# Performance work log

Hardware: AMD Instinct MI355X
Metric: run time of the kernel (lower is better)

Reference implementation:

```python
import jax, jax.numpy as jnp
import numpy as np

B, T, C = 2, 2048, 2048
N_HEAD, N_KV_HEAD, HEAD_DIM = 16, 4, 128
N_REP = N_HEAD // N_KV_HEAD
EPS = 1e-05


def setup_inputs() -> dict:
    key = jax.random.key(0)
    ks = jax.random.split(key, 8)
    # rope freqs as cos/sin of theta_t,i = t / 10000^(2i/d)
    inv_freq = 1.0 / (10000.0 ** (np.arange(0, HEAD_DIM, 2, dtype=np.float32) / HEAD_DIM))
    ang = np.arange(T, dtype=np.float32)[:, None] * inv_freq[None, :]  # [T, HEAD_DIM//2]
    scale = 0.02
    return {
        "x": jax.random.normal(ks[0], (B, T, C), jnp.float32),
        "freqs_cos": jnp.asarray(np.cos(ang)),
        "freqs_sin": jnp.asarray(np.sin(ang)),
        "wq": jax.random.normal(ks[1], (C, N_HEAD * HEAD_DIM), jnp.float32) * scale,
        "wk": jax.random.normal(ks[2], (C, N_KV_HEAD * HEAD_DIM), jnp.float32) * scale,
        "wv": jax.random.normal(ks[3], (C, N_KV_HEAD * HEAD_DIM), jnp.float32) * scale,
        "wo": jax.random.normal(ks[4], (N_HEAD * HEAD_DIM, C), jnp.float32) * scale,
        "q_norm_w": jnp.ones((HEAD_DIM,), jnp.float32),
        "k_norm_w": jnp.ones((HEAD_DIM,), jnp.float32),
    }


def _rmsnorm(x, w):
    var = jnp.mean(jnp.square(x), axis=-1, keepdims=True)
    return x * jax.lax.rsqrt(var + EPS) * w


def _rope(x, cos, sin):
    # x: [B, T, H, D]; interpret last dim as interleaved (real, imag) pairs
    xr = x[..., 0::2]
    xi = x[..., 1::2]
    c = cos[None, :, None, :]
    s = sin[None, :, None, :]
    out_r = xr * c - xi * s
    out_i = xr * s + xi * c
    return jnp.stack([out_r, out_i], axis=-1).reshape(x.shape)


def reference(x, freqs_cos, freqs_sin, wq, wk, wv, wo, q_norm_w, k_norm_w):
    # QKV projections
    xq = (x @ wq).reshape(B, T, N_HEAD, HEAD_DIM)
    xk = (x @ wk).reshape(B, T, N_KV_HEAD, HEAD_DIM)
    xv = (x @ wv).reshape(B, T, N_KV_HEAD, HEAD_DIM)
    # optional q/k RMSNorm (use_qk_norm=True)
    xq = _rmsnorm(xq, q_norm_w)
    xk = _rmsnorm(xk, k_norm_w)
    # RoPE
    xq = _rope(xq, freqs_cos, freqs_sin)
    xk = _rope(xk, freqs_cos, freqs_sin)
    # GQA expand: each kv head repeated N_REP times contiguously
    xk = jnp.repeat(xk, N_REP, axis=2)  # [B, T, N_HEAD, D]
    xv = jnp.repeat(xv, N_REP, axis=2)
    # causal SDPA
    scores = jnp.einsum("bthd,bshd->bhts", xq, xk) / jnp.sqrt(jnp.float32(HEAD_DIM))
    causal = jnp.tril(jnp.ones((T, T), bool))
    scores = jnp.where(causal[None, None], scores, jnp.float32(-1e30))
    attn = jax.nn.softmax(scores, axis=-1)
    y = jnp.einsum("bhts,bshd->bthd", attn, xv).reshape(B, T, N_HEAD * HEAD_DIM)
    return y @ wo
```

## Files before the change

### kernel.cpp

```cpp
#include <hip/hip_runtime.h>
#include <hip/hip_bf16.h>

using u16 = unsigned short;
using u32 = unsigned int;

typedef short bf16x8 __attribute__((ext_vector_type(8)));
typedef float f32x4 __attribute__((ext_vector_type(4)));

#define AS1 __attribute__((address_space(1)))
#define AS3 __attribute__((address_space(3)))

__device__ __forceinline__ void gll16(const void* g, void* l) {
  __builtin_amdgcn_global_load_lds((const AS1 u32*)g, (AS3 u32*)l, 16, 0, 0);
}

__device__ __forceinline__ u16 f2bf(float x) {
  u32 u = __builtin_bit_cast(u32, x);
  u32 r = (u + 0x7fffu + ((u >> 16) & 1u)) >> 16;
  return (u16)r;
}
__device__ __forceinline__ u32 pk2(float lo, float hi) {
  return (u32)f2bf(lo) | ((u32)f2bf(hi) << 16);
}
__device__ __forceinline__ u16 f2bf_fast(float x) {
  __hip_bfloat16 h = __float2bfloat16(x);
  return __builtin_bit_cast(u16, h);
}

__device__ __forceinline__ void trans64(const float* __restrict__ in, u16* __restrict__ out,
                                        int R, int Cc, int bx, int by, float (*tl)[65]) {
  int c0 = bx * 64, r0 = by * 64, tid = threadIdx.x;
#pragma unroll
  for (int i = 0; i < 16; i++) {
    int idx = i * 256 + tid; int tr = idx >> 6, tc = idx & 63;
    tl[tr][tc] = in[(size_t)(r0 + tr) * Cc + c0 + tc];
  }
  __syncthreads();
#pragma unroll
  for (int i = 0; i < 16; i++) {
    int idx = i * 256 + tid; int tr = idx >> 6, tc = idx & 63;
    out[(size_t)(c0 + tr) * R + r0 + tc] = f2bf(tl[tc][tr]);
  }
}

__global__ void k_prep(const float* __restrict__ x, u16* __restrict__ xb,
                       const float* __restrict__ wq, u16* __restrict__ wqt,
                       const float* __restrict__ wk, const float* __restrict__ wv,
                       u16* __restrict__ wkvt,
                       const float* __restrict__ wo, u16* __restrict__ wot,
                       const float* __restrict__ fc, const float* __restrict__ fs,
                       float2* __restrict__ fcs) {
  __shared__ float tl[64][65];
  int gid = blockIdx.x;
  if (gid < 4096) {
    int i = gid * 256 + threadIdx.x;
    const float4* p = (const float4*)(x + (size_t)i * 8);
    float4 a = p[0], b = p[1];
    uint4 o;
    o.x = pk2(a.x, a.y); o.y = pk2(a.z, a.w);
    o.z = pk2(b.x, b.y); o.w = pk2(b.z, b.w);
    *(uint4*)(xb + (size_t)i * 8) = o;
  } else if (gid < 5120) {
    int t = gid - 4096; trans64(wq, wqt, 2048, 2048, t & 31, t >> 5, tl);
  } else if (gid < 5376) {
    int t = gid - 5120; trans64(wk, wkvt, 2048, 512, t & 7, t >> 3, tl);
  } else if (gid < 5632) {
    int t = gid - 5376; trans64(wv, wkvt + 512 * 2048, 2048, 512, t & 7, t >> 3, tl);
  } else if (gid < 6656) {
    int t = gid - 5632; trans64(wo, wot, 2048, 2048, t & 31, t >> 5, tl);
  } else {
    int base = (gid - 6656) * 2048 + threadIdx.x * 8;
#pragma unroll
    for (int j = 0; j < 8; j++) {
      int idx = base + j;
      fcs[idx] = make_float2(fc[idx], fs[idx]);
    }
  }
}

__global__ __launch_bounds__(512, 2) void k_gemm_qkv(
    const u16* __restrict__ A, const u16* __restrict__ BT0, const u16* __restrict__ BT1,
    u16* __restrict__ Qout, u16* __restrict__ Kout, u16* __restrict__ Vout,
    const float* __restrict__ nwq, const float* __restrict__ nwk,
    const float2* __restrict__ fcs) {
  __shared__ char lds[147456];
  const int K = 2048;
  int tid = threadIdx.x, w = tid >> 6, l = tid & 63, lg = l >> 4, ll = l & 15;
  int bid = blockIdx.x;

  if (bid < 256) {
    int wr = w >> 2, wc = w & 3;
    int xcd = bid & 7, r = bid >> 3;
    int colg = xcd & 1, rowg = xcd >> 1;
    int bxt = colg * 4 + (r & 3);
    int bm0 = (rowg * 8 + (r >> 2)) * 128;
    int bn0 = bxt * 256;

    auto stage = [&](int si, int kt) {
      char* Sb = lds + si * 49152;
      int k0 = kt * 64;
#pragma unroll
      for (int i = 0; i < 2; i++) {
        int base = i * 512 + (w << 6);
        int c = base + l;
        int row = c >> 3, kc = (c & 7) ^ (row & 7);
        gll16(A + (size_t)(bm0 + row) * K + k0 + kc * 8, Sb + base * 16);
      }
#pragma unroll
      for (int i = 0; i < 4; i++) {
        int base = i * 512 + (w << 6);
        int c = base + l;
        int row = c >> 3, kc = (c & 7) ^ (row & 7);
        gll16(BT0 + (size_t)(bn0 + row) * K + k0 + kc * 8, Sb + 16384 + base * 16);
      }
    };

    f32x4 acc[4][4] = {};
    stage(0, 0); stage(1, 1);
    asm volatile("s_waitcnt vmcnt(6)" ::: "memory");
    __builtin_amdgcn_s_barrier();
    __builtin_amdgcn_sched_barrier(0);

    for (int kt = 0; kt < 32; ++kt) {
      int cs = kt % 3;
      if (kt + 2 < 32) stage((kt + 2) % 3, kt + 2);
      char* As = lds + cs * 49152;
      char* Bs = As + 16384;
      __builtin_amdgcn_s_setprio(1);
#pragma unroll
      for (int ks = 0; ks < 2; ks++) {
        bf16x8 af[4], bf[4];
#pragma unroll
        for (int m = 0; m < 4; m++) {
          int row = 64 * wr + 16 * m + ll;
          af[m] = *(const bf16x8*)(As + row * 128 + (((lg + 4 * ks) ^ (row & 7)) << 4));
        }
#pragma unroll
        for (int n = 0; n < 4; n++) {
          int row = 64 * wc + 16 * n + ll;
          bf[n] = *(const bf16x8*)(Bs + row * 128 + (((lg + 4 * ks) ^ (row & 7)) << 4));
        }
#pragma unroll
        for (int m = 0; m < 4; m++)
#pragma unroll
          for (int n = 0; n < 4; n++)
            acc[m][n] = __builtin_amdgcn_mfma_f32_16x16x32_bf16(af[m], bf[n], acc[m][n], 0, 0, 0);
      }
      __builtin_amdgcn_s_setprio(0);
      if (kt + 2 < 32) {
        asm volatile("s_waitcnt vmcnt(6)" ::: "memory");
      } else {
        asm volatile("s_waitcnt vmcnt(0)" ::: "memory");
      }
      __builtin_amdgcn_s_barrier();
      __builtin_amdgcn_sched_barrier(0);
    }

    float* ssum = (float*)lds;
    float ps[4][4];
#pragma unroll
    for (int m = 0; m < 4; m++)
#pragma unroll
      for (int r2 = 0; r2 < 4; r2++) {
        float p = 0.f;
#pragma unroll
        for (int n = 0; n < 4; n++) p += acc[m][n][r2] * acc[m][n][r2];
#pragma unroll
        for (int msk = 1; msk < 16; msk <<= 1) p += __shfl_xor(p, msk);
        ps[m][r2] = p;
      }
    if (ll == 0) {
#pragma unroll
      for (int m = 0; m < 4; m++)
#pragma unroll
        for (int r2 = 0; r2 < 4; r2++)
          ssum[wr * 256 + (16 * m + 4 * lg + r2) * 4 + wc] = ps[m][r2];
    }
    __syncthreads();
    int pbase = (wc < 2) ? 0 : 2;
    float rs[4][4];
#pragma unroll
    for (int m = 0; m < 4; m++)
#pragma unroll
      for (int r2 = 0; r2 < 4; r2++) {
        int rowl = 16 * m + 4 * lg + r2;
        const float* sp = ssum + wr * 256 + rowl * 4;
        float tot = sp[pbase] + sp[pbase + 1];
        rs[m][r2] = rsqrtf(tot * (1.0f / 128.0f) + 1e-5f) * 0.12751744843f;
      }
#pragma unroll
    for (int m = 0; m < 4; m++)
#pragma unroll
      for (int n = 0; n < 4; n++) {
        int col = bn0 + 64 * wc + 16 * n + ll;
        int d = col & 127;
        float wgt = nwq[d];
        int i = d >> 1;
#pragma unroll
        for (int r2 = 0; r2 < 4; r2++) {
          int row = bm0 + 64 * wr + 16 * m + 4 * lg + r2;
          int t = row & 2047;
          float y = acc[m][n][r2] * rs[m][r2] * wgt;
          float p = __shfl_xor(y, 1);
          float2 cs2 = fcs[t * 64 + i];
          float o = (ll & 1) ? (p * cs2.y + y * cs2.x) : (y * cs2.x - p * cs2.y);
          Qout[(size_t)row * 2048 + col] = f2bf(o);
        }
      }
  } else {
    int wr = w >> 2, wc = w & 3;
    int lid = bid - 256;
    int xcd = lid & 7, r = lid >> 3;
    int colg = xcd & 1, rowg = xcd >> 1;
    int bxt = colg * 4 + (r & 3);
    int bm0 = (rowg * 8 + (r >> 2)) * 128;
    int bn0 = bxt * 128;
    bool kpath = (bn0 < 512);

    auto stage = [&](int si, int kt) {
      char* Sb = lds + si * 32768;
      int k0 = kt * 64;
#pragma unroll
      for (int i = 0; i < 2; i++) {
        int base = i * 512 + (w << 6);
        int c = base + l;
        int row = c >> 3, kc = (c & 7) ^ (row & 7);
        gll16(A + (size_t)(bm0 + row) * K + k0 + kc * 8, Sb + base * 16);
        gll16(BT1 + (size_t)(bn0 + row) * K + k0 + kc * 8, Sb + 16384 + base * 16);
      }
    };

    f32x4 acc[4][2] = {};
    stage(0, 0); stage(1, 1); stage(2, 2);
    asm volatile("s_waitcnt vmcnt(8)" ::: "memory");
    __builtin_amdgcn_s_barrier();
    __builtin_amdgcn_sched_barrier(0);

    for (int kt = 0; kt < 32; ++kt) {
      int cs = kt & 3;
      if (kt + 3 < 32) stage((kt + 3) & 3, kt + 3);
      char* As = lds + cs * 32768;
      char* Bs = As + 16384;
      __builtin_amdgcn_s_setprio(1);
#pragma unroll
      for (int ks = 0; ks < 2; ks++) {
        bf16x8 af[4], bf[2];
#pragma unroll
        for (int m = 0; m < 4; m++) {
          int row = 64 * wr + 16 * m + ll;
          af[m] = *(const bf16x8*)(As + row * 128 + (((lg + 4 * ks) ^ (row & 7)) << 4));
        }
#pragma unroll
        for (int n = 0; n < 2; n++) {
          int row = 32 * wc + 16 * n + ll;
          bf[n] = *(const bf16x8*)(Bs + row * 128 + (((lg + 4 * ks) ^ (row & 7)) << 4));
        }
#pragma unroll
        for (int m = 0; m < 4; m++)
#pragma unroll
          for (int n = 0; n < 2; n++)
            acc[m][n] = __builtin_amdgcn_mfma_f32_16x16x32_bf16(af[m], bf[n], acc[m][n], 0, 0, 0);
      }
      __builtin_amdgcn_s_setprio(0);
      if (kt <= 28) {
        asm volatile("s_waitcnt vmcnt(8)" ::: "memory");
      } else if (kt == 29) {
        asm volatile("s_waitcnt vmcnt(4)" ::: "memory");
      } else {
        asm volatile("s_waitcnt vmcnt(0)" ::: "memory");
      }
      __builtin_amdgcn_s_barrier();
      __builtin_amdgcn_sched_barrier(0);
    }

    if (kpath) {
      float* ssum = (float*)lds;
      float ps[4][4];
#pragma unroll
      for (int m = 0; m < 4; m++)
#pragma unroll
        for (int r2 = 0; r2 < 4; r2++) {
          float p = 0.f;
#pragma unroll
          for (int n = 0; n < 2; n++) p += acc[m][n][r2] * acc[m][n][r2];
#pragma unroll
          for (int msk = 1; msk < 16; msk <<= 1) p += __shfl_xor(p, msk);
          ps[m][r2] = p;
        }
      if (ll == 0) {
#pragma unroll
        for (int m = 0; m < 4; m++)
#pragma unroll
          for (int r2 = 0; r2 < 4; r2++)
            ssum[wr * 256 + (16 * m + 4 * lg + r2) * 4 + wc] = ps[m][r2];
      }
      __syncthreads();
      float rs[4][4];
#pragma unroll
      for (int m = 0; m < 4; m++)
#pragma unroll
        for (int r2 = 0; r2 < 4; r2++) {
          int rowl = 16 * m + 4 * lg + r2;
          const float* sp = ssum + wr * 256 + rowl * 4;
          float tot = sp[0] + sp[1] + sp[2] + sp[3];
          rs[m][r2] = rsqrtf(tot * (1.0f / 128.0f) + 1e-5f);
        }
#pragma unroll
      for (int m = 0; m < 4; m++)
#pragma unroll
        for (int n = 0; n < 2; n++) {
          int col = bn0 + 32 * wc + 16 * n + ll;
          int d = col & 127;
          float wgt = nwk[d];
          int i = d >> 1;
#pragma unroll
          for (int r2 = 0; r2 < 4; r2++) {
            int row = bm0 + 64 * wr + 16 * m + 4 * lg + r2;
            int t = row & 2047;
            float y = acc[m][n][r2] * rs[m][r2] * wgt;
            float p = __shfl_xor(y, 1);
            float2 cs2 = fcs[t * 64 + i];
            float o = (ll & 1) ? (p * cs2.y + y * cs2.x) : (y * cs2.x - p * cs2.y);
            Kout[(size_t)row * 512 + col] = f2bf(o);
          }
        }
    } else {
      int b = bm0 >> 11, t0g = bm0 & 2047;
      int kvh = (bn0 - 512) >> 7;
      int bk = b * 4 + kvh;
#pragma unroll
      for (int m = 0; m < 4; m++)
#pragma unroll
        for (int n = 0; n < 2; n++) {
          int d = 32 * wc + 16 * n + ll;
          int tloc = 64 * wr + 16 * m + 4 * lg;
          u32 w0 = pk2(acc[m][n][0], acc[m][n][1]);
          u32 w1 = pk2(acc[m][n][2], acc[m][n][3]);
          int byte = (d * 256 + tloc * 2) ^ ((d & 7) << 4);
          *(uint2*)(lds + byte) = make_uint2(w0, w1);
        }
      __syncthreads();
      int tc = tid & 15, dbase = tid >> 4;
#pragma unroll
      for (int pass = 0; pass < 4; pass++) {
        int d = dbase + pass * 32;
        int byte = (d * 256 + tc * 16) ^ ((d & 7) << 4);
        uint4 v = *(const uint4*)(lds + byte);
        *(uint4*)(Vout + ((size_t)(bk * 128 + d)) * 2048 + t0g + tc * 8) = v;
      }
    }
  }
}

__global__ __launch_bounds__(512, 2) void k_gemm_o(
    const u16* __restrict__ A, const u16* __restrict__ BT, float* __restrict__ C) {
  __shared__ char lds[147456];
  const int K = 2048;
  int tid = threadIdx.x, w = tid >> 6, l = tid & 63, lg = l >> 4, ll = l & 15;
  int wr = w >> 2, wc = w & 3;
  int lid = blockIdx.y * 8 + blockIdx.x;
  int xcd = lid & 7, r = lid >> 3;
  int colg = xcd & 1, rowg = xcd >> 1;
  int bxt = colg * 4 + (r & 3);
  int bm0 = (rowg * 8 + (r >> 2)) * 128;
  int bn0 = bxt * 256;

  auto stage = [&](int si, int kt) {
    char* Sb = lds + si * 49152;
    int k0 = kt * 64;
#pragma unroll
    for (int i = 0; i < 2; i++) {
      int base = i * 512 + (w << 6);
      int c = base + l;
      int row = c >> 3, kc = (c & 7) ^ (row & 7);
      gll16(A + (size_t)(bm0 + row) * K + k0 + kc * 8, Sb + base * 16);
    }
#pragma unroll
    for (int i = 0; i < 4; i++) {
      int base = i * 512 + (w << 6);
      int c = base + l;
      int row = c >> 3, kc = (c & 7) ^ (row & 7);
      gll16(BT + (size_t)(bn0 + row) * K + k0 + kc * 8, Sb + 16384 + base * 16);
    }
  };

  f32x4 acc[4][4] = {};
  stage(0, 0); stage(1, 1);
  asm volatile("s_waitcnt vmcnt(6)" ::: "memory");
  __builtin_amdgcn_s_barrier();
  __builtin_amdgcn_sched_barrier(0);

  for (int kt = 0; kt < 32; ++kt) {
    int cs = kt % 3;
    if (kt + 2 < 32) stage((kt + 2) % 3, kt + 2);
    char* As = lds + cs * 49152;
    char* Bs = As + 16384;
    __builtin_amdgcn_s_setprio(1);
#pragma unroll
    for (int ks = 0; ks < 2; ks++) {
      bf16x8 af[4], bf[4];
#pragma unroll
      for (int m = 0; m < 4; m++) {
        int row = 64 * wr + 16 * m + ll;
        af[m] = *(const bf16x8*)(As + row * 128 + (((lg + 4 * ks) ^ (row & 7)) << 4));
      }
#pragma unroll
      for (int n = 0; n < 4; n++) {
        int row = 64 * wc + 16 * n + ll;
        bf[n] = *(const bf16x8*)(Bs + row * 128 + (((lg + 4 * ks) ^ (row & 7)) << 4));
      }
#pragma unroll
      for (int m = 0; m < 4; m++)
#pragma unroll
        for (int n = 0; n < 4; n++)
          acc[m][n] = __builtin_amdgcn_mfma_f32_16x16x32_bf16(af[m], bf[n], acc[m][n], 0, 0, 0);
    }
    __builtin_amdgcn_s_setprio(0);
    if (kt + 2 < 32) {
      asm volatile("s_waitcnt vmcnt(6)" ::: "memory");
    } else {
      asm volatile("s_waitcnt vmcnt(0)" ::: "memory");
    }
    __builtin_amdgcn_s_barrier();
    __builtin_amdgcn_sched_barrier(0);
  }

#pragma unroll
  for (int m = 0; m < 4; m++)
#pragma unroll
    for (int n = 0; n < 4; n++) {
      int row = bm0 + 64 * wr + 16 * m + 4 * lg;
      int col = bn0 + 64 * wc + 16 * n + ll;
      float* cp = C + (size_t)row * 2048 + col;
#pragma unroll
      for (int r2 = 0; r2 < 4; r2++) cp[(size_t)r2 * 2048] = acc[m][n][r2];
    }
}

__global__ __launch_bounds__(512, 2) void k_attn(
    const u16* __restrict__ Q, const u16* __restrict__ Kb,
    const u16* __restrict__ Vt, u16* __restrict__ Y) {
  __shared__ char lds[81920];
  char* Ps = lds + 65536;
  int tid = threadIdx.x, w = tid >> 6, l = tid & 63, lg = l >> 4, ll = l & 15;
  int fid = blockIdx.x;
  int g = fid & 7, rank = fid >> 3;
  int b = g >> 2, kvh = g & 3;
  int h = kvh * 4 + (w & 3);
  int rgrp = w >> 2;
  const u16* Kbase = Kb + ((size_t)b * 2048) * 512 + kvh * 128;
  const u16* Vbase = Vt + ((size_t)(b * 4 + kvh) * 128) * 2048;

  const bf16x8 vones = {(short)0x3F80, (short)0x3F80, (short)0x3F80, (short)0x3F80,
                        (short)0x3F80, (short)0x3F80, (short)0x3F80, (short)0x3F80};

  auto stage = [&](int bi, int k0) {
    char* Kd = lds + (bi ? 32768 : 0);
    char* Vd = Kd + 16384;
#pragma unroll
    for (int i = 0; i < 2; i++) {
      int base = i * 512 + (w << 6);
      int c = base + l;
      int dst = base * 16;
      int krow = c >> 4, ksrc = (c & 15) ^ (krow & 7);
      gll16(Kbase + (size_t)(k0 + krow) * 512 + ksrc * 8, Kd + dst);
      int vd = c >> 3, vsrc = (c & 7) ^ (vd & 7);
      gll16(Vbase + (size_t)vd * 2048 + k0 + vsrc * 8, Vd + dst);
    }
  };

#pragma unroll 1
  for (int qi = 0; qi < 2; qi++) {
    int qt = qi ? (63 - rank) : rank;
    int q0 = qt * 32;
    int nt = (qt >> 1) + 1;
    bf16x8 qf[4];
    {
      int qrow = b * 2048 + q0 + rgrp * 16 + ll;
      const u16* qp = Q + (size_t)qrow * 2048 + h * 128;
#pragma unroll
      for (int ks = 0; ks < 4; ks++) qf[ks] = *(const bf16x8*)(qp + ks * 32 + lg * 8);
    }
    f32x4 o[8] = {};
    f32x4 lacc = {};

    stage(0, 0);
    asm volatile("s_waitcnt vmcnt(0)" ::: "memory");
    __syncthreads();

    int cur = 0;
    for (int it = 0; it < nt; ++it) {
      if (it + 1 < nt) stage(cur ^ 1, (it + 1) * 64);
      char* Ks = lds + (cur ? 32768 : 0);
      char* Vs = Ks + 16384;
      f32x4 s[4] = {};
      __builtin_amdgcn_s_setprio(1);
#pragma unroll
      for (int ks = 0; ks < 4; ks++) {
#pragma unroll
        for (int n = 0; n < 4; n++) {
          int row = 16 * n + ll;
          bf16x8 kf = *(const bf16x8*)(Ks + ((row * 256 + (lg + 4 * ks) * 16) ^ ((row & 7) << 4)));
          s[n] = __builtin_amdgcn_mfma_f32_16x16x32_bf16(qf[ks], kf, s[n], 0, 0, 0);
        }
      }
      __builtin_amdgcn_s_setprio(0);
      if (it == nt - 1) {
        int k0 = it * 64;
#pragma unroll
        for (int n = 0; n < 4; n++) {
          int kk = k0 + 16 * n + ll;
#pragma unroll
          for (int r = 0; r < 4; r++) {
            int qq = q0 + rgrp * 16 + 4 * lg + r;
            if (kk > qq) s[n][r] = -1e30f;
          }
        }
      }
#pragma unroll
      for (int r = 0; r < 4; r++) {
        int prow = 4 * lg + r;
#pragma unroll
        for (int n = 0; n < 4; n++) {
          float e = exp2f(s[n][r]);
          int byte = (w << 11) + ((prow * 128 + (16 * n + ll) * 2) ^ ((prow & 7) << 4));
          *(u16*)(Ps + byte) = f2bf_fast(e);
        }
      }
      __builtin_amdgcn_s_setprio(1);
#pragma unroll
      for (int ks = 0; ks < 2; ks++) {
        bf16x8 pf = *(const bf16x8*)(Ps + (w << 11) + ((ll * 128 + (lg + 4 * ks) * 16) ^ ((ll & 7) << 4)));
        lacc = __builtin_amdgcn_mfma_f32_16x16x32_bf16(pf, vones, lacc, 0, 0, 0);
#pragma unroll
        for (int n = 0; n < 8; n++) {
          int row = 16 * n + ll;
          bf16x8 vf = *(const bf16x8*)(Vs + ((row * 128 + (lg + 4 * ks) * 16) ^ ((row & 7) << 4)));
          o[n] = __builtin_amdgcn_mfma_f32_16x16x32_bf16(pf, vf, o[n], 0, 0, 0);
        }
      }
      __builtin_amdgcn_s_setprio(0);
      asm volatile("s_waitcnt vmcnt(0)" ::: "memory");
      __syncthreads();
      cur ^= 1;
    }
    float rl[4];
#pragma unroll
    for (int r = 0; r < 4; r++) rl[r] = 1.0f / lacc[r];
#pragma unroll
    for (int n = 0; n < 8; n++) {
      int col = h * 128 + 16 * n + ll;
#pragma unroll
      for (int r = 0; r < 4; r++) {
        int trow = b * 2048 + q0 + rgrp * 16 + 4 * lg + r;
        Y[(size_t)trow * 2048 + col] = f2bf_fast(o[n][r] * rl[r]);
      }
    }
  }
}

extern "C" void kernel_launch(void* const* d_in, const int* in_sizes, int n_in,
                              void* d_out, int out_size, void* d_ws, size_t ws_size,
                              hipStream_t stream) {
  const float* x   = (const float*)d_in[0];
  const float* fc  = (const float*)d_in[1];
  const float* fs  = (const float*)d_in[2];
  const float* wq  = (const float*)d_in[3];
  const float* wk  = (const float*)d_in[4];
  const float* wv  = (const float*)d_in[5];
  const float* wo  = (const float*)d_in[6];
  const float* qnw = (const float*)d_in[7];
  const float* knw = (const float*)d_in[8];
  float* out = (float*)d_out;

  const size_t MB = 1ull << 20;
  char* ws = (char*)d_ws;
  u16*    xb   = (u16*)(ws);
  u16*    wqt  = (u16*)(ws + 16 * MB);
  u16*    wkvt = (u16*)(ws + 24 * MB);
  u16*    wot  = (u16*)(ws + 28 * MB);
  u16*    Qb   = (u16*)(ws + 36 * MB);
  u16*    Kbq  = (u16*)(ws + 52 * MB);
  u16*    Vtg  = (u16*)(ws + 56 * MB);
  u16*    Yb   = (u16*)(ws + 60 * MB);
  float2* fcs  = (float2*)(ws + 76 * MB);

  hipLaunchKernelGGL(k_prep, dim3(6720), dim3(256), 0, stream,
                     x, xb, wq, wqt, wk, wv, wkvt, wo, wot, fc, fs, fcs);
  hipLaunchKernelGGL(k_gemm_qkv, dim3(512), dim3(512), 0, stream,
                     xb, wqt, wkvt, Qb, Kbq, Vtg, qnw, knw, fcs);
  hipLaunchKernelGGL(k_attn, dim3(256), dim3(512), 0, stream, Qb, Kbq, Vtg, Yb);
  hipLaunchKernelGGL(k_gemm_o, dim3(8, 32), dim3(512), 0, stream, Yb, wot, out);
}
```

Measured before the change: 186.4 us.

## Restructure attention to 4-wave blocks with 32-row per-wave Q tiles

```diff
diff --git a/kernel.cpp b/kernel.cpp
--- a/kernel.cpp
+++ b/kernel.cpp
@@ -437,29 +437,44 @@
     }
 }
 
-__global__ __launch_bounds__(512, 2) void k_attn(
+__global__ __launch_bounds__(256, 2) void k_attn(
     const u16* __restrict__ Q, const u16* __restrict__ Kb,
     const u16* __restrict__ Vt, u16* __restrict__ Y) {
-  __shared__ char lds[81920];
+  __shared__ char lds[73728];
   char* Ps = lds + 65536;
   int tid = threadIdx.x, w = tid >> 6, l = tid & 63, lg = l >> 4, ll = l & 15;
   int fid = blockIdx.x;
-  int g = fid & 7, rank = fid >> 3;
+  int g = fid & 7;
   int b = g >> 2, kvh = g & 3;
-  int h = kvh * 4 + (w & 3);
-  int rgrp = w >> 2;
+  int hp = (fid >> 3) & 1;
+  int qt = 31 - (fid >> 4);
+  int h = kvh * 4 + hp * 2 + (w & 1);
+  int rgrp = w >> 1;
+  int q0 = qt * 64;
+  int nt = qt + 1;
   const u16* Kbase = Kb + ((size_t)b * 2048) * 512 + kvh * 128;
   const u16* Vbase = Vt + ((size_t)(b * 4 + kvh) * 128) * 2048;
 
   const bf16x8 vones = {(short)0x3F80, (short)0x3F80, (short)0x3F80, (short)0x3F80,
                         (short)0x3F80, (short)0x3F80, (short)0x3F80, (short)0x3F80};
+
+  bf16x8 qf[2][4];
+#pragma unroll
+  for (int m = 0; m < 2; m++) {
+    int qrow = b * 2048 + q0 + rgrp * 32 + m * 16 + ll;
+    const u16* qp = Q + (size_t)qrow * 2048 + h * 128;
+#pragma unroll
+    for (int ks = 0; ks < 4; ks++) qf[m][ks] = *(const bf16x8*)(qp + ks * 32 + lg * 8);
+  }
+  f32x4 o[2][8] = {};
+  f32x4 lacc[2] = {};
 
   auto stage = [&](int bi, int k0) {
     char* Kd = lds + (bi ? 32768 : 0);
     char* Vd = Kd + 16384;
 #pragma unroll
-    for (int i = 0; i < 2; i++) {
-      int base = i * 512 + (w << 6);
+    for (int i = 0; i < 4; i++) {
+      int base = i * 256 + (w << 6);
       int c = base + l;
       int dst = base * 16;
       int krow = c >> 4, ksrc = (c & 15) ^ (krow & 7);
@@ -469,91 +484,92 @@
     }
   };
 
-#pragma unroll 1
-  for (int qi = 0; qi < 2; qi++) {
-    int qt = qi ? (63 - rank) : rank;
-    int q0 = qt * 32;
-    int nt = (qt >> 1) + 1;
-    bf16x8 qf[4];
-    {
-      int qrow = b * 2048 + q0 + rgrp * 16 + ll;
-      const u16* qp = Q + (size_t)qrow * 2048 + h * 128;
-#pragma unroll
-      for (int ks = 0; ks < 4; ks++) qf[ks] = *(const bf16x8*)(qp + ks * 32 + lg * 8);
-    }
-    f32x4 o[8] = {};
-    f32x4 lacc = {};
-
-    stage(0, 0);
+  stage(0, 0);
+  asm volatile("s_waitcnt vmcnt(0)" ::: "memory");
+  __syncthreads();
+
+  int cur = 0;
+  for (int it = 0; it < nt; ++it) {
+    if (it + 1 < nt) stage(cur ^ 1, (it + 1) * 64);
+    char* Ks = lds + (cur ? 32768 : 0);
+    char* Vs = Ks + 16384;
+    f32x4 s[2][4] = {};
+    __builtin_amdgcn_s_setprio(1);
+#pragma unroll
+    for (int ks = 0; ks < 4; ks++) {
+#pragma unroll
+      for (int n = 0; n < 4; n++) {
+        int row = 16 * n + ll;
+        bf16x8 kf = *(const bf16x8*)(Ks + ((row * 256 + (lg + 4 * ks) * 16) ^ ((row & 7) << 4)));
+        s[0][n] = __builtin_amdgcn_mfma_f32_16x16x32_bf16(qf[0][ks], kf, s[0][n], 0, 0, 0);
+        s[1][n] = __builtin_amdgcn_mfma_f32_16x16x32_bf16(qf[1][ks], kf, s[1][n], 0, 0, 0);
+      }
+    }
+    __builtin_amdgcn_s_setprio(0);
+    if (it == nt - 1) {
+      int k0 = it * 64;
+#pragma unroll
+      for (int m = 0; m < 2; m++)
+#pragma unroll
+        for (int n = 0; n < 4; n++) {
+          int kk = k0 + 16 * n + ll;
+#pragma unroll
+          for (int r = 0; r < 4; r++) {
+            int qq = q0 + rgrp * 32 + m * 16 + 4 * lg + r;
+            if (kk > qq) s[m][n][r] = -1e30f;
+          }
+        }
+    }
+#pragma unroll
+    for (int hs = 0; hs < 2; hs++) {
+#pragma unroll
+      for (int m = 0; m < 2; m++)
+#pragma unroll
+        for (int r = 0; r < 4; r++) {
+          int prow = m * 16 + 4 * lg + r;
+          int swz = ((prow >> 2) & 3) << 4;
+#pragma unroll
+          for (int nn = 0; nn < 2; nn++) {
+            int n = 2 * hs + nn;
+            float e = exp2f(s[m][n][r]);
+            int lcol = 16 * nn + ll;
+            int byte = (w << 11) + ((prow * 64 + lcol * 2) ^ swz);
+            *(u16*)(Ps + byte) = f2bf_fast(e);
+          }
+        }
+      __builtin_amdgcn_s_setprio(1);
+      bf16x8 pfm[2];
+#pragma unroll
+      for (int m = 0; m < 2; m++) {
+        int prow = m * 16 + ll;
+        pfm[m] = *(const bf16x8*)(Ps + (w << 11) + ((prow * 64 + lg * 16) ^ (((prow >> 2) & 3) << 4)));
+        lacc[m] = __builtin_amdgcn_mfma_f32_16x16x32_bf16(pfm[m], vones, lacc[m], 0, 0, 0);
+      }
+#pragma unroll
+      for (int n = 0; n < 8; n++) {
+        int row = 16 * n + ll;
+        bf16x8 vf = *(const bf16x8*)(Vs + ((row * 128 + (lg + 4 * hs) * 16) ^ ((row & 7) << 4)));
+        o[0][n] = __builtin_amdgcn_mfma_f32_16x16x32_bf16(pfm[0], vf, o[0][n], 0, 0, 0);
+        o[1][n] = __builtin_amdgcn_mfma_f32_16x16x32_bf16(pfm[1], vf, o[1][n], 0, 0, 0);
+      }
+      __builtin_amdgcn_s_setprio(0);
+    }
     asm volatile("s_waitcnt vmcnt(0)" ::: "memory");
     __syncthreads();
-
-    int cur = 0;
-    for (int it = 0; it < nt; ++it) {
-      if (it + 1 < nt) stage(cur ^ 1, (it + 1) * 64);
-      char* Ks = lds + (cur ? 32768 : 0);
-      char* Vs = Ks + 16384;
-      f32x4 s[4] = {};
-      __builtin_amdgcn_s_setprio(1);
-#pragma unroll
-      for (int ks = 0; ks < 4; ks++) {
-#pragma unroll
-        for (int n = 0; n < 4; n++) {
-          int row = 16 * n + ll;
-          bf16x8 kf = *(const bf16x8*)(Ks + ((row * 256 + (lg + 4 * ks) * 16) ^ ((row & 7) << 4)));
-          s[n] = __builtin_amdgcn_mfma_f32_16x16x32_bf16(qf[ks], kf, s[n], 0, 0, 0);
-        }
-      }
-      __builtin_amdgcn_s_setprio(0);
-      if (it == nt - 1) {
-        int k0 = it * 64;
-#pragma unroll
-        for (int n = 0; n < 4; n++) {
-          int kk = k0 + 16 * n + ll;
-#pragma unroll
-          for (int r = 0; r < 4; r++) {
-            int qq = q0 + rgrp * 16 + 4 * lg + r;
-            if (kk > qq) s[n][r] = -1e30f;
-          }
-        }
-      }
-#pragma unroll
-      for (int r = 0; r < 4; r++) {
-        int prow = 4 * lg + r;
-#pragma unroll
-        for (int n = 0; n < 4; n++) {
-          float e = exp2f(s[n][r]);
-          int byte = (w << 11) + ((prow * 128 + (16 * n + ll) * 2) ^ ((prow & 7) << 4));
-          *(u16*)(Ps + byte) = f2bf_fast(e);
-        }
-      }
-      __builtin_amdgcn_s_setprio(1);
-#pragma unroll
-      for (int ks = 0; ks < 2; ks++) {
-        bf16x8 pf = *(const bf16x8*)(Ps + (w << 11) + ((ll * 128 + (lg + 4 * ks) * 16) ^ ((ll & 7) << 4)));
-        lacc = __builtin_amdgcn_mfma_f32_16x16x32_bf16(pf, vones, lacc, 0, 0, 0);
-#pragma unroll
-        for (int n = 0; n < 8; n++) {
-          int row = 16 * n + ll;
-          bf16x8 vf = *(const bf16x8*)(Vs + ((row * 128 + (lg + 4 * ks) * 16) ^ ((row & 7) << 4)));
-          o[n] = __builtin_amdgcn_mfma_f32_16x16x32_bf16(pf, vf, o[n], 0, 0, 0);
-        }
-      }
-      __builtin_amdgcn_s_setprio(0);
-      asm volatile("s_waitcnt vmcnt(0)" ::: "memory");
-      __syncthreads();
-      cur ^= 1;
-    }
+    cur ^= 1;
+  }
+#pragma unroll
+  for (int m = 0; m < 2; m++) {
     float rl[4];
 #pragma unroll
-    for (int r = 0; r < 4; r++) rl[r] = 1.0f / lacc[r];
+    for (int r = 0; r < 4; r++) rl[r] = 1.0f / lacc[m][r];
 #pragma unroll
     for (int n = 0; n < 8; n++) {
       int col = h * 128 + 16 * n + ll;
 #pragma unroll
       for (int r = 0; r < 4; r++) {
-        int trow = b * 2048 + q0 + rgrp * 16 + 4 * lg + r;
-        Y[(size_t)trow * 2048 + col] = f2bf_fast(o[n][r] * rl[r]);
+        int trow = b * 2048 + q0 + rgrp * 32 + m * 16 + 4 * lg + r;
+        Y[(size_t)trow * 2048 + col] = f2bf_fast(o[m][n][r] * rl[r]);
       }
     }
   }
@@ -589,6 +605,6 @@
                      x, xb, wq, wqt, wk, wv, wkvt, wo, wot, fc, fs, fcs);
   hipLaunchKernelGGL(k_gemm_qkv, dim3(512), dim3(512), 0, stream,
                      xb, wqt, wkvt, Qb, Kbq, Vtg, qnw, knw, fcs);
-  hipLaunchKernelGGL(k_attn, dim3(256), dim3(512), 0, stream, Qb, Kbq, Vtg, Yb);
+  hipLaunchKernelGGL(k_attn, dim3(512), dim3(256), 0, stream, Qb, Kbq, Vtg, Yb);
   hipLaunchKernelGGL(k_gemm_o, dim3(8, 32), dim3(512), 0, stream, Yb, wot, out);
 }
```

New measurement: 197.4 us. +5.9%, slower.
